# Kernel optimization log

Measured on AMD Instinct MI355X. Metric: run time of the kernel, lower is better.

Reference implementation:

```python
import jax, jax.numpy as jnp
import numpy as np

D_MODEL = 1024
N_HEADS = 16
D_K = D_MODEL // N_HEADS

def setup_inputs() -> dict:
    key = jax.random.key(0)
    ks = jax.random.split(key, 11)
    B, S = 2, 2048
    s = 1.0 / np.sqrt(D_MODEL)
    inp = {
        'Q': jax.random.normal(ks[0], (B, S, D_MODEL), jnp.float32),
        'K': jax.random.normal(ks[1], (B, S, D_MODEL), jnp.float32),
        'V': jax.random.normal(ks[2], (B, S, D_MODEL), jnp.float32),
        'Wq': jax.random.normal(ks[3], (D_MODEL, D_MODEL), jnp.float32) * s,
        'bq': jnp.zeros((D_MODEL,), jnp.float32),
        'Wk': jax.random.normal(ks[4], (D_MODEL, D_MODEL), jnp.float32) * s,
        'bk': jnp.zeros((D_MODEL,), jnp.float32),
        'Wv': jax.random.normal(ks[5], (D_MODEL, D_MODEL), jnp.float32) * s,
        'bv': jnp.zeros((D_MODEL,), jnp.float32),
        'Wo': jax.random.normal(ks[6], (D_MODEL, D_MODEL), jnp.float32) * s,
        'bo': jnp.zeros((D_MODEL,), jnp.float32),
    }
    return inp

def _split_heads(x):
    B, S, _ = x.shape
    return x.reshape(B, S, N_HEADS, D_K).transpose(0, 2, 1, 3)  # [B,H,S,dk]

def reference(Q, K, V, Wq, bq, Wk, bk, Wv, bv, Wo, bo):
    q = _split_heads(Q @ Wq.T + bq)
    k = _split_heads(K @ Wk.T + bk)
    v = _split_heads(V @ Wv.T + bv)
    scores = jnp.einsum('bhqd,bhkd->bhqk', q, k) / jnp.sqrt(jnp.asarray(D_K, q.dtype))
    attn_weights = jax.nn.softmax(scores, axis=-1)          # [B,H,S,S]
    attn_out = jnp.einsum('bhqk,bhkd->bhqd', attn_weights, v)
    B, H, S, dk = attn_out.shape
    attn_out = attn_out.transpose(0, 2, 1, 3).reshape(B, S, H * dk)
    out = attn_out @ Wo.T + bo
    return (out, attn_weights)
```

## Files before the change

kernel.cpp:

```cpp
#include <hip/hip_runtime.h>
#include <hip/hip_bf16.h>
#include <math.h>


typedef __bf16 bf16;
typedef __bf16 bf16x8 __attribute__((ext_vector_type(8)));
typedef float  f32x4  __attribute__((ext_vector_type(4)));

#define GLDS16(gp, lp) __builtin_amdgcn_global_load_lds(                     \
    (const __attribute__((address_space(1))) void*)(gp),                     \
    (__attribute__((address_space(3))) void*)(lp), 16, 0, 0)

static __device__ __forceinline__ bf16x8 cvt8(const f32x4 lo, const f32x4 hi) {
    bf16x8 r;
    r[0] = (bf16)lo[0]; r[1] = (bf16)lo[1]; r[2] = (bf16)lo[2]; r[3] = (bf16)lo[3];
    r[4] = (bf16)hi[0]; r[5] = (bf16)hi[1]; r[6] = (bf16)hi[2]; r[7] = (bf16)hi[3];
    return r;
}

template<int MODE>
__global__ __launch_bounds__(256)
void gemm_bt(const void* __restrict__ A0v, const void* __restrict__ A1v, const void* __restrict__ A2v,
             const float* __restrict__ W0, const float* __restrict__ W1, const float* __restrict__ W2,
             const float* __restrict__ B0, const float* __restrict__ B1, const float* __restrict__ B2,
             void* __restrict__ O0v, void* __restrict__ O1v, void* __restrict__ O2v)
{
    __shared__ __align__(16) float AsF[128 * 32];
    __shared__ __align__(16) float BsF[128 * 32];
    bf16* AsH = (bf16*)AsF;

    const int tid  = threadIdx.x;
    const int lane = tid & 63;
    const int w    = tid >> 6;
    const int wr   = w >> 1, wc = w & 1;
    const int g    = lane >> 4, c = lane & 15;

    const int mb  = blockIdx.x, nb = blockIdx.y;
    const int mat = (MODE == 1) ? (nb >> 3) : 0;
    const int nbi = (MODE == 1) ? (nb & 7) : nb;

    const float* Af = (MODE == 1)
        ? (mat == 0 ? (const float*)A0v : (mat == 1 ? (const float*)A1v : (const float*)A2v))
        : nullptr;
    const bf16*  Ah = (MODE == 0) ? (const bf16*)A0v : nullptr;
    const float* W  = (MODE == 1) ? (mat == 0 ? W0 : (mat == 1 ? W1 : W2)) : W0;
    const float* Bi = (MODE == 1) ? (mat == 0 ? B0 : (mat == 1 ? B1 : B2)) : B0;

    const size_t m0 = (size_t)mb * 128;
    const int    n0 = nbi * 128;

    f32x4 acc[4][4];
#pragma unroll
    for (int i = 0; i < 4; i++)
#pragma unroll
        for (int j = 0; j < 4; j++) acc[i][j] = (f32x4){0.f, 0.f, 0.f, 0.f};

    for (int k0 = 0; k0 < 1024; k0 += 32) {
        __syncthreads();
        if constexpr (MODE == 1) {
#pragma unroll
            for (int s = 0; s < 4; s++) {
                const int ca  = w * 4 + s;
                const int row = ca * 8 + (lane >> 3);
                const int pos = lane & 7;
                const float* ga = Af + (size_t)(m0 + row) * 1024 + k0 + ((pos ^ (row & 7)) << 2);
                GLDS16(ga, &AsF[ca * 256]);
            }
        } else {
#pragma unroll
            for (int s = 0; s < 2; s++) {
                const int ca  = w * 2 + s;
                const int row = ca * 16 + (lane >> 2);
                const int pos = lane & 3;
                const bf16* ga = Ah + (size_t)(m0 + row) * 1024 + k0 + ((pos ^ ((row >> 1) & 3)) << 3);
                GLDS16(ga, &AsH[ca * 512]);
            }
        }
#pragma unroll
        for (int s = 0; s < 4; s++) {
            const int cb  = w * 4 + s;
            const int row = cb * 8 + (lane >> 3);
            const int pos = lane & 7;
            const float* gb = W + (size_t)(n0 + row) * 1024 + k0 + ((pos ^ (row & 7)) << 2);
            GLDS16(gb, &BsF[cb * 256]);
        }
        __syncthreads();

        bf16x8 av[4], bv[4];
#pragma unroll
        for (int i = 0; i < 4; i++) {
            const int row = wr * 64 + i * 16 + c;
            if constexpr (MODE == 1) {
                const int s7 = row & 7;
                const f32x4 lo = *(const f32x4*)&AsF[row * 32 + (((2 * g)     ^ s7) << 2)];
                const f32x4 hi = *(const f32x4*)&AsF[row * 32 + (((2 * g + 1) ^ s7) << 2)];
                av[i] = cvt8(lo, hi);
            } else {
                av[i] = *(const bf16x8*)&AsH[row * 32 + ((g ^ ((row >> 1) & 3)) << 3)];
            }
        }
#pragma unroll
        for (int j = 0; j < 4; j++) {
            const int row = wc * 64 + j * 16 + c;
            const int s7  = row & 7;
            const f32x4 lo = *(const f32x4*)&BsF[row * 32 + (((2 * g)     ^ s7) << 2)];
            const f32x4 hi = *(const f32x4*)&BsF[row * 32 + (((2 * g + 1) ^ s7) << 2)];
            bv[j] = cvt8(lo, hi);
        }
#pragma unroll
        for (int i = 0; i < 4; i++)
#pragma unroll
            for (int j = 0; j < 4; j++)
                acc[i][j] = __builtin_amdgcn_mfma_f32_16x16x32_bf16(av[i], bv[j], acc[i][j], 0, 0, 0);
    }

#pragma unroll
    for (int j = 0; j < 4; j++) {
        const int   nl   = wc * 64 + j * 16 + c;
        const int   n    = n0 + nl;
        const float bval = Bi[n];
#pragma unroll
        for (int i = 0; i < 4; i++) {
#pragma unroll
            for (int r = 0; r < 4; r++) {
                const size_t m   = m0 + wr * 64 + i * 16 + g * 4 + r;
                const float  val = acc[i][j][r] + bval;
                if (MODE == 0) {
                    ((float*)O0v)[m * 1024 + n] = val;
                } else {
                    const bf16 ob = (bf16)val;
                    const int  bb = (int)(m >> 11), s = (int)(m & 2047);
                    const int  hh = n >> 6, d = n & 63;
                    if (mat < 2) {
                        bf16* Oqk = (mat == 0) ? (bf16*)O0v : (bf16*)O1v;
                        Oqk[(((size_t)bb * 16 + hh) * 2048 + s) * 64 + d] = ob;
                    } else {
                        ((bf16*)O2v)[(((size_t)bb * 16 + hh) * 64 + d) * 2048 + s] = ob;
                    }
                }
            }
        }
    }
}

__global__ __launch_bounds__(256, 4)
void attn_kernel(const bf16* __restrict__ Qh, const bf16* __restrict__ Kh,
                 const bf16* __restrict__ VhT, float* __restrict__ PW,
                 bf16* __restrict__ AO)
{
    __shared__ __align__(16) bf16 Ks[2 * 64 * 64];
    __shared__ __align__(16) bf16 Vs[2 * 64 * 64];
    __shared__ __align__(16) bf16 Ps[64 * 64];

    const int tid  = threadIdx.x;
    const int lane = tid & 63;
    const int w    = tid >> 6;
    const int g    = lane >> 4, c = lane & 15;

    const int L   = blockIdx.x;
    const int swz = (L & 7) * 128 + (L >> 3);
    const int bh  = swz >> 5;
    const int qb  = swz & 31;

    const bf16* qp = Qh + (((size_t)bh * 2048) + qb * 64) * 64;
    const bf16* kp = Kh + ((size_t)bh * 2048) * 64;
    const bf16* vp = VhT + ((size_t)bh * 64) * 2048;
    float*      pw = PW + (size_t)bh * 2048 * 2048 + (size_t)(qb * 64) * 2048;

    bf16x8 aq[2];
#pragma unroll
    for (int kk = 0; kk < 2; kk++)
        aq[kk] = *(const bf16x8*)(qp + (w * 16 + c) * 64 + kk * 32 + g * 8);

    const float SC = 0.18033688011112042f;

    const int srow = (lane >> 3);
    const int spos = lane & 7;

    float lr[4] = {0.f, 0.f, 0.f, 0.f};
#pragma unroll
    for (int s2 = 0; s2 < 2; s2++) {
        const int cs = w * 2 + s2, row = cs * 8 + srow;
        GLDS16(kp + (size_t)row * 64 + ((spos ^ (row & 7)) << 3), &Ks[cs * 512]);
    }
    asm volatile("s_waitcnt vmcnt(0)" ::: "memory");
    __builtin_amdgcn_s_barrier();
    asm volatile("" ::: "memory");

    for (int t = 0; t < 32; t++) {
        const bf16* kb = &Ks[(t & 1) * 4096];
        if (t < 31) {
#pragma unroll
            for (int s2 = 0; s2 < 2; s2++) {
                const int cs = w * 2 + s2, row = cs * 8 + srow;
                GLDS16(kp + (size_t)((t + 1) * 64 + row) * 64 + ((spos ^ (row & 7)) << 3),
                       &Ks[((t + 1) & 1) * 4096 + cs * 512]);
            }
        }
        f32x4 sj[4];
#pragma unroll
        for (int j = 0; j < 4; j++) sj[j] = (f32x4){0.f, 0.f, 0.f, 0.f};
#pragma unroll
        for (int kk = 0; kk < 2; kk++) {
#pragma unroll
            for (int j = 0; j < 4; j++) {
                const int row = j * 16 + c;
                const bf16x8 bk = *(const bf16x8*)&kb[row * 64 + (((kk * 4 + g) ^ (row & 7)) << 3)];
                sj[j] = __builtin_amdgcn_mfma_f32_16x16x32_bf16(aq[kk], bk, sj[j], 0, 0, 0);
            }
        }
#pragma unroll
        for (int r = 0; r < 4; r++)
            lr[r] += exp2f(sj[0][r] * SC) + exp2f(sj[1][r] * SC)
                   + exp2f(sj[2][r] * SC) + exp2f(sj[3][r] * SC);

        asm volatile("s_waitcnt vmcnt(0)" ::: "memory");
        __builtin_amdgcn_s_barrier();
        asm volatile("" ::: "memory");
    }

    float inv[4];
#pragma unroll
    for (int r = 0; r < 4; r++) {
        float s = lr[r];
        s += __shfl_xor(s, 1);
        s += __shfl_xor(s, 2);
        s += __shfl_xor(s, 4);
        s += __shfl_xor(s, 8);
        inv[r] = 1.0f / s;
    }

    f32x4 oj[4];
#pragma unroll
    for (int j = 0; j < 4; j++) oj[j] = (f32x4){0.f, 0.f, 0.f, 0.f};

#pragma unroll
    for (int s2 = 0; s2 < 2; s2++) {
        const int cs = w * 2 + s2, row = cs * 8 + srow;
        GLDS16(kp + (size_t)row * 64 + ((spos ^ (row & 7)) << 3), &Ks[cs * 512]);
        GLDS16(vp + (size_t)row * 2048 + ((spos ^ (row & 7)) << 3), &Vs[cs * 512]);
    }
    asm volatile("s_waitcnt vmcnt(0)" ::: "memory");
    __builtin_amdgcn_s_barrier();
    asm volatile("" ::: "memory");

    for (int t = 0; t < 32; t++) {
        const bf16* kb = &Ks[(t & 1) * 4096];
        const bf16* vb = &Vs[(t & 1) * 4096];
        if (t < 31) {
#pragma unroll
            for (int s2 = 0; s2 < 2; s2++) {
                const int cs = w * 2 + s2, row = cs * 8 + srow;
                GLDS16(kp + (size_t)((t + 1) * 64 + row) * 64 + ((spos ^ (row & 7)) << 3),
                       &Ks[((t + 1) & 1) * 4096 + cs * 512]);
                GLDS16(vp + (size_t)row * 2048 + (t + 1) * 64 + ((spos ^ (row & 7)) << 3),
                       &Vs[((t + 1) & 1) * 4096 + cs * 512]);
            }
        }
        f32x4 sj[4];
#pragma unroll
        for (int j = 0; j < 4; j++) sj[j] = (f32x4){0.f, 0.f, 0.f, 0.f};
#pragma unroll
        for (int kk = 0; kk < 2; kk++) {
#pragma unroll
            for (int j = 0; j < 4; j++) {
                const int row = j * 16 + c;
                const bf16x8 bk = *(const bf16x8*)&kb[row * 64 + (((kk * 4 + g) ^ (row & 7)) << 3)];
                sj[j] = __builtin_amdgcn_mfma_f32_16x16x32_bf16(aq[kk], bk, sj[j], 0, 0, 0);
            }
        }
#pragma unroll
        for (int j = 0; j < 4; j++) {
#pragma unroll
            for (int r = 0; r < 4; r++) {
                const float p   = exp2f(sj[j][r] * SC) * inv[r];
                const int   row = w * 16 + g * 4 + r;
                const int   col = j * 16 + c;
                __builtin_nontemporal_store(p, &pw[(size_t)row * 2048 + t * 64 + col]);
                Ps[row * 64 + (((col >> 3) ^ (row & 7)) << 3) + (col & 7)] = (bf16)p;
            }
        }
#pragma unroll
        for (int kk = 0; kk < 2; kk++) {
            const int prow = w * 16 + c;
            const bf16x8 ap = *(const bf16x8*)&Ps[prow * 64 + (((kk * 4 + g) ^ (prow & 7)) << 3)];
#pragma unroll
            for (int j = 0; j < 4; j++) {
                const int vrow = j * 16 + c;
                const bf16x8 bvv = *(const bf16x8*)&vb[vrow * 64 + (((kk * 4 + g) ^ (vrow & 7)) << 3)];
                oj[j] = __builtin_amdgcn_mfma_f32_16x16x32_bf16(ap, bvv, oj[j], 0, 0, 0);
            }
        }
        asm volatile("s_waitcnt vmcnt(16)" ::: "memory");
        __builtin_amdgcn_s_barrier();
        asm volatile("" ::: "memory");
    }

    const int b = bh >> 4, h = bh & 15;
#pragma unroll
    for (int j = 0; j < 4; j++) {
#pragma unroll
        for (int r = 0; r < 4; r++) {
            const size_t m = (size_t)b * 2048 + qb * 64 + w * 16 + g * 4 + r;
            const int    n = h * 64 + j * 16 + c;
            AO[m * 1024 + n] = (bf16)oj[j][r];
        }
    }
}

extern "C" void kernel_launch(void* const* d_in, const int* in_sizes, int n_in,
                              void* d_out, int out_size, void* d_ws, size_t ws_size,
                              hipStream_t stream)
{
    const float* Q  = (const float*)d_in[0];
    const float* K  = (const float*)d_in[1];
    const float* V  = (const float*)d_in[2];
    const float* Wq = (const float*)d_in[3];
    const float* bq = (const float*)d_in[4];
    const float* Wk = (const float*)d_in[5];
    const float* bk = (const float*)d_in[6];
    const float* Wv = (const float*)d_in[7];
    const float* bv = (const float*)d_in[8];
    const float* Wo = (const float*)d_in[9];
    const float* bo = (const float*)d_in[10];

    float* outf  = (float*)d_out;
    float* attnw = outf + (size_t)4096 * 1024;

    bf16* qws  = (bf16*)d_ws;
    bf16* kws  = qws + (size_t)4096 * 1024;
    bf16* vws  = kws + (size_t)4096 * 1024;
    bf16* aows = vws + (size_t)4096 * 1024;

    gemm_bt<1><<<dim3(32, 24), 256, 0, stream>>>(Q, K, V, Wq, Wk, Wv, bq, bk, bv, qws, kws, vws);
    attn_kernel<<<dim3(1024), 256, 0, stream>>>(qws, kws, vws, attnw, aows);
    gemm_bt<0><<<dim3(32, 8), 256, 0, stream>>>(aows, nullptr, nullptr, Wo, nullptr, nullptr,
                                                bo, nullptr, nullptr, outf, nullptr, nullptr);
}
```

Baseline: 290.5 us.

## Pre-convert fp32 inputs and weights to bf16 before the projection GEMMs

Adds a conversion kernel that casts Q, K, V and all four weight matrices to bf16 in the workspace. A new GEMM variant then loads bf16 tiles for both operands, which halves LDS and global traffic per tile and drops the per-iteration fp32-to-bf16 conversions in the inner loop. This path runs only when the workspace is at least 64 MB; otherwise the old fp32-loading GEMM is used. The trade-off is an extra pass over about 56 MB of fp32 data plus the bf16 writes, and one more kernel launch.

```diff
diff --git a/kernel.cpp b/kernel.cpp
--- a/kernel.cpp
+++ b/kernel.cpp
@@ -18,16 +18,41 @@
     return r;
 }
 
+__global__ __launch_bounds__(256)
+void cvt7(const float* __restrict__ s0, const float* __restrict__ s1, const float* __restrict__ s2,
+          const float* __restrict__ s3, const float* __restrict__ s4, const float* __restrict__ s5,
+          const float* __restrict__ s6,
+          bf16* __restrict__ d0, bf16* __restrict__ d1, bf16* __restrict__ d2,
+          bf16* __restrict__ d3, bf16* __restrict__ d4, bf16* __restrict__ d5,
+          bf16* __restrict__ d6)
+{
+    const int seg = blockIdx.y;
+    const float* s; bf16* d; int n;
+    switch (seg) {
+        case 0: s = s0; d = d0; n = 4194304; break;
+        case 1: s = s1; d = d1; n = 4194304; break;
+        case 2: s = s2; d = d2; n = 4194304; break;
+        case 3: s = s3; d = d3; n = 1048576; break;
+        case 4: s = s4; d = d4; n = 1048576; break;
+        case 5: s = s5; d = d5; n = 1048576; break;
+        default: s = s6; d = d6; n = 1048576; break;
+    }
+    const size_t i = ((size_t)blockIdx.x * 256 + threadIdx.x) * 8;
+    if (i >= (size_t)n) return;
+    const f32x4 lo = *(const f32x4*)(s + i);
+    const f32x4 hi = *(const f32x4*)(s + i + 4);
+    *(bf16x8*)(d + i) = cvt8(lo, hi);
+}
+
 template<int MODE>
 __global__ __launch_bounds__(256)
-void gemm_bt(const void* __restrict__ A0v, const void* __restrict__ A1v, const void* __restrict__ A2v,
-             const float* __restrict__ W0, const float* __restrict__ W1, const float* __restrict__ W2,
+void gemm_bb(const bf16* __restrict__ A0, const bf16* __restrict__ A1, const bf16* __restrict__ A2,
+             const bf16* __restrict__ W0, const bf16* __restrict__ W1, const bf16* __restrict__ W2,
              const float* __restrict__ B0, const float* __restrict__ B1, const float* __restrict__ B2,
              void* __restrict__ O0v, void* __restrict__ O1v, void* __restrict__ O2v)
 {
-    __shared__ __align__(16) float AsF[128 * 32];
-    __shared__ __align__(16) float BsF[128 * 32];
-    bf16* AsH = (bf16*)AsF;
+    __shared__ __align__(16) bf16 As[128 * 32];
+    __shared__ __align__(16) bf16 Bs[128 * 32];
 
     const int tid  = threadIdx.x;
     const int lane = tid & 63;
@@ -39,11 +64,8 @@
     const int mat = (MODE == 1) ? (nb >> 3) : 0;
     const int nbi = (MODE == 1) ? (nb & 7) : nb;
 
-    const float* Af = (MODE == 1)
-        ? (mat == 0 ? (const float*)A0v : (mat == 1 ? (const float*)A1v : (const float*)A2v))
-        : nullptr;
-    const bf16*  Ah = (MODE == 0) ? (const bf16*)A0v : nullptr;
-    const float* W  = (MODE == 1) ? (mat == 0 ? W0 : (mat == 1 ? W1 : W2)) : W0;
+    const bf16*  A  = (MODE == 1) ? (mat == 0 ? A0 : (mat == 1 ? A1 : A2)) : A0;
+    const bf16*  W  = (MODE == 1) ? (mat == 0 ? W0 : (mat == 1 ? W1 : W2)) : W0;
     const float* Bi = (MODE == 1) ? (mat == 0 ? B0 : (mat == 1 ? B1 : B2)) : B0;
 
     const size_t m0 = (size_t)mb * 128;
@@ -55,34 +77,19 @@
 #pragma unroll
         for (int j = 0; j < 4; j++) acc[i][j] = (f32x4){0.f, 0.f, 0.f, 0.f};
 
+    const int srow = lane >> 2;
+    const int spos = lane & 3;
+
     for (int k0 = 0; k0 < 1024; k0 += 32) {
         __syncthreads();
-        if constexpr (MODE == 1) {
-#pragma unroll
-            for (int s = 0; s < 4; s++) {
-                const int ca  = w * 4 + s;
-                const int row = ca * 8 + (lane >> 3);
-                const int pos = lane & 7;
-                const float* ga = Af + (size_t)(m0 + row) * 1024 + k0 + ((pos ^ (row & 7)) << 2);
-                GLDS16(ga, &AsF[ca * 256]);
-            }
-        } else {
-#pragma unroll
-            for (int s = 0; s < 2; s++) {
-                const int ca  = w * 2 + s;
-                const int row = ca * 16 + (lane >> 2);
-                const int pos = lane & 3;
-                const bf16* ga = Ah + (size_t)(m0 + row) * 1024 + k0 + ((pos ^ ((row >> 1) & 3)) << 3);
-                GLDS16(ga, &AsH[ca * 512]);
-            }
-        }
-#pragma unroll
-        for (int s = 0; s < 4; s++) {
-            const int cb  = w * 4 + s;
-            const int row = cb * 8 + (lane >> 3);
-            const int pos = lane & 7;
-            const float* gb = W + (size_t)(n0 + row) * 1024 + k0 + ((pos ^ (row & 7)) << 2);
-            GLDS16(gb, &BsF[cb * 256]);
+#pragma unroll
+        for (int s = 0; s < 2; s++) {
+            const int ca  = w * 2 + s;
+            const int row = ca * 16 + srow;
+            GLDS16(A + (size_t)(m0 + row) * 1024 + k0 + ((spos ^ ((row >> 1) & 3)) << 3),
+                   &As[ca * 512]);
+            GLDS16(W + (size_t)(n0 + row) * 1024 + k0 + ((spos ^ ((row >> 1) & 3)) << 3),
+                   &Bs[ca * 512]);
         }
         __syncthreads();
 
@@ -90,22 +97,12 @@
 #pragma unroll
         for (int i = 0; i < 4; i++) {
             const int row = wr * 64 + i * 16 + c;
-            if constexpr (MODE == 1) {
-                const int s7 = row & 7;
-                const f32x4 lo = *(const f32x4*)&AsF[row * 32 + (((2 * g)     ^ s7) << 2)];
-                const f32x4 hi = *(const f32x4*)&AsF[row * 32 + (((2 * g + 1) ^ s7) << 2)];
-                av[i] = cvt8(lo, hi);
-            } else {
-                av[i] = *(const bf16x8*)&AsH[row * 32 + ((g ^ ((row >> 1) & 3)) << 3)];
-            }
+            av[i] = *(const bf16x8*)&As[row * 32 + ((g ^ ((row >> 1) & 3)) << 3)];
         }
 #pragma unroll
         for (int j = 0; j < 4; j++) {
             const int row = wc * 64 + j * 16 + c;
-            const int s7  = row & 7;
-            const f32x4 lo = *(const f32x4*)&BsF[row * 32 + (((2 * g)     ^ s7) << 2)];
-            const f32x4 hi = *(const f32x4*)&BsF[row * 32 + (((2 * g + 1) ^ s7) << 2)];
-            bv[j] = cvt8(lo, hi);
+            bv[j] = *(const bf16x8*)&Bs[row * 32 + ((g ^ ((row >> 1) & 3)) << 3)];
         }
 #pragma unroll
         for (int i = 0; i < 4; i++)
@@ -143,6 +140,128 @@
     }
 }
 
+template<int MODE>
+__global__ __launch_bounds__(256)
+void gemm_bt(const void* __restrict__ A0v, const void* __restrict__ A1v, const void* __restrict__ A2v,
+             const float* __restrict__ W0, const float* __restrict__ W1, const float* __restrict__ W2,
+             const float* __restrict__ B0, const float* __restrict__ B1, const float* __restrict__ B2,
+             void* __restrict__ O0v, void* __restrict__ O1v, void* __restrict__ O2v)
+{
+    __shared__ __align__(16) float AsF[128 * 32];
+    __shared__ __align__(16) float BsF[128 * 32];
+    bf16* AsH = (bf16*)AsF;
+
+    const int tid  = threadIdx.x;
+    const int lane = tid & 63;
+    const int w    = tid >> 6;
+    const int wr   = w >> 1, wc = w & 1;
+    const int g    = lane >> 4, c = lane & 15;
+
+    const int mb  = blockIdx.x, nb = blockIdx.y;
+    const int mat = (MODE == 1) ? (nb >> 3) : 0;
+    const int nbi = (MODE == 1) ? (nb & 7) : nb;
+
+    const float* Af = (MODE == 1)
+        ? (mat == 0 ? (const float*)A0v : (mat == 1 ? (const float*)A1v : (const float*)A2v))
+        : nullptr;
+    const bf16*  Ah = (MODE == 0) ? (const bf16*)A0v : nullptr;
+    const float* W  = (MODE == 1) ? (mat == 0 ? W0 : (mat == 1 ? W1 : W2)) : W0;
+    const float* Bi = (MODE == 1) ? (mat == 0 ? B0 : (mat == 1 ? B1 : B2)) : B0;
+
+    const size_t m0 = (size_t)mb * 128;
+    const int    n0 = nbi * 128;
+
+    f32x4 acc[4][4];
+#pragma unroll
+    for (int i = 0; i < 4; i++)
+#pragma unroll
+        for (int j = 0; j < 4; j++) acc[i][j] = (f32x4){0.f, 0.f, 0.f, 0.f};
+
+    for (int k0 = 0; k0 < 1024; k0 += 32) {
+        __syncthreads();
+        if constexpr (MODE == 1) {
+#pragma unroll
+            for (int s = 0; s < 4; s++) {
+                const int ca  = w * 4 + s;
+                const int row = ca * 8 + (lane >> 3);
+                const int pos = lane & 7;
+                GLDS16(Af + (size_t)(m0 + row) * 1024 + k0 + ((pos ^ (row & 7)) << 2), &AsF[ca * 256]);
+            }
+        } else {
+#pragma unroll
+            for (int s = 0; s < 2; s++) {
+                const int ca  = w * 2 + s;
+                const int row = ca * 16 + (lane >> 2);
+                const int pos = lane & 3;
+                GLDS16(Ah + (size_t)(m0 + row) * 1024 + k0 + ((pos ^ ((row >> 1) & 3)) << 3), &AsH[ca * 512]);
+            }
+        }
+#pragma unroll
+        for (int s = 0; s < 4; s++) {
+            const int cb  = w * 4 + s;
+            const int row = cb * 8 + (lane >> 3);
+            const int pos = lane & 7;
+            GLDS16(W + (size_t)(n0 + row) * 1024 + k0 + ((pos ^ (row & 7)) << 2), &BsF[cb * 256]);
+        }
+        __syncthreads();
+
+        bf16x8 av[4], bv[4];
+#pragma unroll
+        for (int i = 0; i < 4; i++) {
+            const int row = wr * 64 + i * 16 + c;
+            if constexpr (MODE == 1) {
+                const int s7 = row & 7;
+                const f32x4 lo = *(const f32x4*)&AsF[row * 32 + (((2 * g)     ^ s7) << 2)];
+                const f32x4 hi = *(const f32x4*)&AsF[row * 32 + (((2 * g + 1) ^ s7) << 2)];
+                av[i] = cvt8(lo, hi);
+            } else {
+                av[i] = *(const bf16x8*)&AsH[row * 32 + ((g ^ ((row >> 1) & 3)) << 3)];
+            }
+        }
+#pragma unroll
+        for (int j = 0; j < 4; j++) {
+            const int row = wc * 64 + j * 16 + c;
+            const int s7  = row & 7;
+            const f32x4 lo = *(const f32x4*)&BsF[row * 32 + (((2 * g)     ^ s7) << 2)];
+            const f32x4 hi = *(const f32x4*)&BsF[row * 32 + (((2 * g + 1) ^ s7) << 2)];
+            bv[j] = cvt8(lo, hi);
+        }
+#pragma unroll
+        for (int i = 0; i < 4; i++)
+#pragma unroll
+            for (int j = 0; j < 4; j++)
+                acc[i][j] = __builtin_amdgcn_mfma_f32_16x16x32_bf16(av[i], bv[j], acc[i][j], 0, 0, 0);
+    }
+
+#pragma unroll
+    for (int j = 0; j < 4; j++) {
+        const int   nl   = wc * 64 + j * 16 + c;
+        const int   n    = n0 + nl;
+        const float bval = Bi[n];
+#pragma unroll
+        for (int i = 0; i < 4; i++) {
+#pragma unroll
+            for (int r = 0; r < 4; r++) {
+                const size_t m   = m0 + wr * 64 + i * 16 + g * 4 + r;
+                const float  val = acc[i][j][r] + bval;
+                if (MODE == 0) {
+                    ((float*)O0v)[m * 1024 + n] = val;
+                } else {
+                    const bf16 ob = (bf16)val;
+                    const int  bb = (int)(m >> 11), s = (int)(m & 2047);
+                    const int  hh = n >> 6, d = n & 63;
+                    if (mat < 2) {
+                        bf16* Oqk = (mat == 0) ? (bf16*)O0v : (bf16*)O1v;
+                        Oqk[(((size_t)bb * 16 + hh) * 2048 + s) * 64 + d] = ob;
+                    } else {
+                        ((bf16*)O2v)[(((size_t)bb * 16 + hh) * 64 + d) * 2048 + s] = ob;
+                    }
+                }
+            }
+        }
+    }
+}
+
 __global__ __launch_bounds__(256, 4)
 void attn_kernel(const bf16* __restrict__ Qh, const bf16* __restrict__ Kh,
                  const bf16* __restrict__ VhT, float* __restrict__ PW,
@@ -327,13 +446,32 @@
     float* outf  = (float*)d_out;
     float* attnw = outf + (size_t)4096 * 1024;
 
-    bf16* qws  = (bf16*)d_ws;
-    bf16* kws  = qws + (size_t)4096 * 1024;
-    bf16* vws  = kws + (size_t)4096 * 1024;
-    bf16* aows = vws + (size_t)4096 * 1024;
-
-    gemm_bt<1><<<dim3(32, 24), 256, 0, stream>>>(Q, K, V, Wq, Wk, Wv, bq, bk, bv, qws, kws, vws);
-    attn_kernel<<<dim3(1024), 256, 0, stream>>>(qws, kws, vws, attnw, aows);
-    gemm_bt<0><<<dim3(32, 8), 256, 0, stream>>>(aows, nullptr, nullptr, Wo, nullptr, nullptr,
-                                                bo, nullptr, nullptr, outf, nullptr, nullptr);
-}
+    bf16* ws   = (bf16*)d_ws;
+    bf16* qws  = ws;
+    bf16* kws  = ws + 4194304;
+    bf16* vws  = ws + 8388608;
+    bf16* aows = ws + 12582912;
+
+    if (ws_size >= 67108864) {
+        bf16* Qb  = ws + 16777216;
+        bf16* Kb  = ws + 20971520;
+        bf16* Vb  = ws + 25165824;
+        bf16* Wqb = ws + 29360128;
+        bf16* Wkb = ws + 30408704;
+        bf16* Wvb = ws + 31457280;
+        bf16* Wob = ws + 32505856;
+
+        cvt7<<<dim3(2048, 7), 256, 0, stream>>>(Q, K, V, Wq, Wk, Wv, Wo,
+                                                Qb, Kb, Vb, Wqb, Wkb, Wvb, Wob);
+        gemm_bb<1><<<dim3(32, 24), 256, 0, stream>>>(Qb, Kb, Vb, Wqb, Wkb, Wvb,
+                                                     bq, bk, bv, qws, kws, vws);
+        attn_kernel<<<dim3(1024), 256, 0, stream>>>(qws, kws, vws, attnw, aows);
+        gemm_bb<0><<<dim3(32, 8), 256, 0, stream>>>(aows, nullptr, nullptr, Wob, nullptr, nullptr,
+                                                    bo, nullptr, nullptr, outf, nullptr, nullptr);
+    } else {
+        gemm_bt<1><<<dim3(32, 24), 256, 0, stream>>>(Q, K, V, Wq, Wk, Wv, bq, bk, bv, qws, kws, vws);
+        attn_kernel<<<dim3(1024), 256, 0, stream>>>(qws, kws, vws, attnw, aows);
+        gemm_bt<0><<<dim3(32, 8), 256, 0, stream>>>(aows, nullptr, nullptr, Wo, nullptr, nullptr,
+                                                    bo, nullptr, nullptr, outf, nullptr, nullptr);
+    }
+}
```

Measured after the change: 276.3 us. 1.05x faster.
